# Kernel tuning notes

Measured on AMD Instinct MI355X. Metric: run time of the kernel, lower is better.

## Reference

```python
import jax, jax.numpy as jnp
import numpy as np

B, S, D_MODEL, D_SPACE, N, TOP_K = 4, 2048, 2048, 64, 512, 8


def topk_sparsify(weights, k):
    # weights: [..., N] softmax probs -> keep top-k, renormalize
    topk_vals, topk_idx = jax.lax.top_k(weights, k)
    n = weights.shape[-1]
    one_hot = jax.nn.one_hot(topk_idx, n, dtype=weights.dtype)  # [..., k, N]
    sparse = (one_hot * topk_vals[..., None]).sum(axis=-2)
    return sparse / (sparse.sum(axis=-1, keepdims=True) + 1e-8)


def setup_inputs() -> dict:
    key = jax.random.key(0)
    k1, k2, k3, k4 = jax.random.split(key, 4)
    total = 4 * N + 2 * 256  # fqk + fv + rqk + rv + fknow + rknow
    return {
        "x": jax.random.normal(k1, (B, S, D_MODEL), jnp.float32),
        "W_all": jax.random.normal(k2, (D_MODEL, 6 * D_SPACE), jnp.float32) * 0.02,
        "b_all": jnp.zeros((6 * D_SPACE,), jnp.float32),
        "neuron_emb": jax.random.normal(k3, (total, D_SPACE), jnp.float32) * 0.02,
    }


def reference(x, W_all, b_all, neuron_emb):
    # deterministic=True path: dropout is identity
    emb = neuron_emb / (jnp.linalg.norm(neuron_emb, axis=-1, keepdims=True) + 1e-8)
    h = jnp.einsum('bsd,de->bse', x, W_all) + b_all  # [B,S,6*d_space]
    hs = jnp.split(h, 6, axis=-1)  # fqk_Q, fqk_K, fv, rqk_Q, rqk_K, rv
    # embedding segments: fqk, fv, rqk, rv (each N wide)
    segs = [emb[0:N], emb[0:N], emb[N:2 * N], emb[2 * N:3 * N], emb[2 * N:3 * N], emb[3 * N:4 * N]]
    prefs = [jax.nn.softmax(jnp.einsum('bsd,nd->bsn', hi, ei), axis=-1)
             for hi, ei in zip(hs, segs)]
    # load-balance aux loss: sum over circuits of N * sum((mean_usage - 1/N)^2)
    target = 1.0 / N
    aux_loss = jnp.float32(0.0)
    for p in prefs:
        usage = p.mean(axis=(0, 1))
        aux_loss = aux_loss + ((usage - target) ** 2).sum() * N
    weights = jnp.stack([topk_sparsify(p, TOP_K) for p in prefs], axis=0)  # [6,B,S,N]
    return weights, aux_loss
```

## Files before the change

### kernel.cpp

```cpp
#include <hip/hip_runtime.h>
#include <hip/hip_bf16.h>
#include <math.h>

#define NC   6
#define NN   512
#define DSP  64
#define MTOK 8192
#define DM   2048
#define HN   384
#define NROWS (NC * MTOK)
#define CAP  2048
#define TAU  2e-4f
#define LGP  17
#define NCPY 16

typedef __attribute__((ext_vector_type(8))) short  bf16x8;
typedef __attribute__((ext_vector_type(4))) float  f32x4;
typedef unsigned short ushort_t;

__device__ __forceinline__ float wsumf(float v) {
#pragma unroll
  for (int m = 32; m >= 1; m >>= 1) v += __shfl_xor(v, m, 64);
  return v;
}
__device__ __forceinline__ double wsumd(double v) {
#pragma unroll
  for (int m = 32; m >= 1; m >>= 1) v += __shfl_xor(v, m, 64);
  return v;
}
__device__ __forceinline__ double wmaxd(double v) {
#pragma unroll
  for (int m = 32; m >= 1; m >>= 1) v = fmax(v, __shfl_xor(v, m, 64));
  return v;
}
__device__ __forceinline__ int wmini(int v) {
#pragma unroll
  for (int m = 32; m >= 1; m >>= 1) v = min(v, __shfl_xor(v, m, 64));
  return v;
}
__device__ __forceinline__ void wmaxf2(float& a, float& b) {
#pragma unroll
  for (int m = 32; m >= 1; m >>= 1) {
    float ta = __shfl_xor(a, m, 64);
    float tb = __shfl_xor(b, m, 64);
    a = fmaxf(a, ta);
    b = fmaxf(b, tb);
  }
}
__device__ __forceinline__ void wsumf2(float& a, float& b) {
#pragma unroll
  for (int m = 32; m >= 1; m >>= 1) {
    float ta = __shfl_xor(a, m, 64);
    float tb = __shfl_xor(b, m, 64);
    a += ta;
    b += tb;
  }
}
__device__ __forceinline__ void bf16split(float f, ushort_t& hi, ushort_t& lo) {
  __hip_bfloat16 hb = __float2bfloat16(f);
  float hf = __bfloat162float(hb);
  __hip_bfloat16 lb = __float2bfloat16(f - hf);
  hi = *(ushort_t*)&hb;
  lo = *(ushort_t*)&lb;
}

__global__ __launch_bounds__(256) void k_norm_emb(const float* __restrict__ emb,
                                                  float* __restrict__ embn32,
                                                  double* __restrict__ embn64) {
  int row  = blockIdx.x * 4 + (threadIdx.x >> 6);
  int lane = threadIdx.x & 63;
  double v = (double)emb[(size_t)row * DSP + lane];
  double ss = wsumd(v * v);
  double inv = 1.0 / (sqrt(ss) + 1e-8);
  double o = v * inv;
  embn64[(size_t)row * DSP + lane] = o;
  embn32[(size_t)row * DSP + lane] = (float)o;
}

__global__ __launch_bounds__(256) void k_split_x(const float* __restrict__ X,
                                                 ushort_t* __restrict__ xhi,
                                                 ushort_t* __restrict__ xlo) {
  const size_t t = (size_t)blockIdx.x * 256 + threadIdx.x;
  const int lane = (int)(t & 63);
  const int s    = (int)((t >> 6) & 63);
  const int g    = (int)(t >> 12);
  const int m = (g << 4) + (lane & 15);
  const int k = (s << 5) + (((lane >> 4) & 3) << 3);
  const float* xp = &X[(size_t)m * DM + k];
  ushort_t h8[8], l8[8];
#pragma unroll
  for (int j = 0; j < 8; j++) bf16split(xp[j], h8[j], l8[j]);
  *(bf16x8*)&xhi[t * 8] = *(bf16x8*)h8;
  *(bf16x8*)&xlo[t * 8] = *(bf16x8*)l8;
}

__global__ __launch_bounds__(256) void k_split_w(const float* __restrict__ W,
                                                 ushort_t* __restrict__ whi,
                                                 ushort_t* __restrict__ wlo) {
  const size_t t = (size_t)blockIdx.x * 256 + threadIdx.x;
  const int lane = (int)(t & 63);
  const int s    = (int)((t >> 6) & 63);
  const int Hb   = (int)(t >> 12);
  const int n = (Hb << 4) + (lane & 15);
  const int k = (s << 5) + (((lane >> 4) & 3) << 3);
  ushort_t h8[8], l8[8];
#pragma unroll
  for (int j = 0; j < 8; j++) bf16split(W[(size_t)(k + j) * HN + n], h8[j], l8[j]);
  *(bf16x8*)&whi[t * 8] = *(bf16x8*)h8;
  *(bf16x8*)&wlo[t * 8] = *(bf16x8*)l8;
}

__global__ __launch_bounds__(256) void k_gemm_mfma(const ushort_t* __restrict__ xhi,
                                                   const ushort_t* __restrict__ xlo,
                                                   const ushort_t* __restrict__ whi,
                                                   const ushort_t* __restrict__ wlo,
                                                   const float* __restrict__ Bv,
                                                   float* __restrict__ H) {
  __shared__ bf16x8 Bs[2][8][64];
  const int tid = threadIdx.x, lane = tid & 63, w = tid >> 6;
  const int Gw  = blockIdx.x * 8 + w * 2;
  const int Hb0 = blockIdx.y * 4;
  const bf16x8* XH = (const bf16x8*)xhi;
  const bf16x8* XL = (const bf16x8*)xlo;
  const bf16x8* WH = (const bf16x8*)whi;
  const bf16x8* WL = (const bf16x8*)wlo;

#define FIDX(G, s) (((size_t)(G) * 64 + (s)) * 64 + lane)

  f32x4 acc[2][4];
#pragma unroll
  for (int i = 0; i < 2; i++)
#pragma unroll
    for (int j = 0; j < 4; j++) acc[i][j] = (f32x4){0.f, 0.f, 0.f, 0.f};

  {
    const int p0 = w, p1 = w + 4;
    Bs[0][p0][lane] = ((p0 & 1) ? WL : WH)[FIDX(Hb0 + (p0 >> 1), 0)];
    Bs[0][p1][lane] = ((p1 & 1) ? WL : WH)[FIDX(Hb0 + (p1 >> 1), 0)];
  }
  __syncthreads();

  for (int s = 0; s < 64; s++) {
    const int buf = s & 1;
    if (s < 63) {
      const int p0 = w, p1 = w + 4, nb = buf ^ 1;
      Bs[nb][p0][lane] = ((p0 & 1) ? WL : WH)[FIDX(Hb0 + (p0 >> 1), s + 1)];
      Bs[nb][p1][lane] = ((p1 & 1) ? WL : WH)[FIDX(Hb0 + (p1 >> 1), s + 1)];
    }
    const bf16x8 ah0 = XH[FIDX(Gw, s)],     al0 = XL[FIDX(Gw, s)];
    const bf16x8 ah1 = XH[FIDX(Gw + 1, s)], al1 = XL[FIDX(Gw + 1, s)];
#pragma unroll
    for (int j = 0; j < 4; j++) {
      const bf16x8 bh = Bs[buf][j * 2][lane];
      const bf16x8 bl = Bs[buf][j * 2 + 1][lane];
      acc[0][j] = __builtin_amdgcn_mfma_f32_16x16x32_bf16(ah0, bh, acc[0][j], 0, 0, 0);
      acc[0][j] = __builtin_amdgcn_mfma_f32_16x16x32_bf16(ah0, bl, acc[0][j], 0, 0, 0);
      acc[0][j] = __builtin_amdgcn_mfma_f32_16x16x32_bf16(al0, bh, acc[0][j], 0, 0, 0);
      acc[1][j] = __builtin_amdgcn_mfma_f32_16x16x32_bf16(ah1, bh, acc[1][j], 0, 0, 0);
      acc[1][j] = __builtin_amdgcn_mfma_f32_16x16x32_bf16(ah1, bl, acc[1][j], 0, 0, 0);
      acc[1][j] = __builtin_amdgcn_mfma_f32_16x16x32_bf16(al1, bh, acc[1][j], 0, 0, 0);
    }
    __syncthreads();
  }

#pragma unroll
  for (int i = 0; i < 2; i++)
#pragma unroll
    for (int j = 0; j < 4; j++) {
      const int col = (Hb0 + j) * 16 + (lane & 15);
      const float bias = Bv[col];
#pragma unroll
      for (int r = 0; r < 4; r++) {
        const int row = (Gw + i) * 16 + ((lane >> 4) << 2) + r;
        H[(size_t)row * HN + col] = acc[i][j][r] + bias;
      }
    }
#undef FIDX
}

__global__ __launch_bounds__(256) void k_split_h(const float* __restrict__ H,
                                                 ushort_t* __restrict__ hfh,
                                                 ushort_t* __restrict__ hfl) {
  const size_t t = (size_t)blockIdx.x * 256 + threadIdx.x;
  const int lane = (int)(t & 63);
  const int ks   = (int)((t >> 6) & 1);
  const int g    = (int)((t >> 7) & 511);
  const int c    = (int)(t >> 16);
  const int m = g * 16 + (lane & 15);
  const int col = c * 64 + ks * 32 + (((lane >> 4) & 3) << 3);
  const float* hp = &H[(size_t)m * HN + col];
  ushort_t h8[8], l8[8];
#pragma unroll
  for (int j = 0; j < 8; j++) bf16split(hp[j], h8[j], l8[j]);
  *(bf16x8*)&hfh[t * 8] = *(bf16x8*)h8;
  *(bf16x8*)&hfl[t * 8] = *(bf16x8*)l8;
}

__global__ __launch_bounds__(256) void k_split_e(const float* __restrict__ E,
                                                 ushort_t* __restrict__ efh,
                                                 ushort_t* __restrict__ efl) {
  const size_t t = (size_t)blockIdx.x * 256 + threadIdx.x;
  const int lane = (int)(t & 63);
  const int ks   = (int)((t >> 6) & 1);
  const int ng   = (int)((t >> 7) & 31);
  const int seg  = (int)(t >> 12);
  const int n = seg * 512 + ng * 16 + (lane & 15);
  const int k = ks * 32 + (((lane >> 4) & 3) << 3);
  const float* ep = &E[(size_t)n * DSP + k];
  ushort_t h8[8], l8[8];
#pragma unroll
  for (int j = 0; j < 8; j++) bf16split(ep[j], h8[j], l8[j]);
  *(bf16x8*)&efh[t * 8] = *(bf16x8*)h8;
  *(bf16x8*)&efl[t * 8] = *(bf16x8*)l8;
}

__global__ __launch_bounds__(512, 3) void k_router_mfma(const ushort_t* __restrict__ hfh,
                                                        const ushort_t* __restrict__ hfl,
                                                        const ushort_t* __restrict__ efh,
                                                        const ushort_t* __restrict__ efl,
                                                        float* __restrict__ OUT,
                                                        float* __restrict__ UC,
                                                        int* __restrict__ ncand,
                                                        int* __restrict__ cand_rows) {
  __shared__ float lgT[NN * LGP];
  const int tid  = threadIdx.x;
  const int lane = tid & 63;
  const int wid  = tid >> 6;
  const int g    = blockIdx.x;
  const int c    = blockIdx.y;
  const int segb = (c <= 1) ? 0 : (c == 2) ? 512 : (c == 5) ? 1536 : 1024;
  const int seg  = segb >> 9;

  const bf16x8* HH = (const bf16x8*)hfh;
  const bf16x8* HL = (const bf16x8*)hfl;
  const bf16x8* EH = (const bf16x8*)efh;
  const bf16x8* EL = (const bf16x8*)efl;

  const size_t ab = ((size_t)(c * 512 + g) * 2) * 64 + lane;
  const bf16x8 ah0 = HH[ab], ah1 = HH[ab + 64];
  const bf16x8 al0 = HL[ab], al1 = HL[ab + 64];

#pragma unroll
  for (int ng = 0; ng < 4; ng++) {
    const int ngg = wid * 4 + ng;
    const size_t bb = ((size_t)(seg * 32 + ngg) * 2) * 64 + lane;
    const bf16x8 bh0 = EH[bb], bh1 = EH[bb + 64];
    const bf16x8 bl0 = EL[bb], bl1 = EL[bb + 64];
    f32x4 a = (f32x4){0.f, 0.f, 0.f, 0.f};
    a = __builtin_amdgcn_mfma_f32_16x16x32_bf16(ah0, bh0, a, 0, 0, 0);
    a = __builtin_amdgcn_mfma_f32_16x16x32_bf16(ah0, bl0, a, 0, 0, 0);
    a = __builtin_amdgcn_mfma_f32_16x16x32_bf16(al0, bh0, a, 0, 0, 0);
    a = __builtin_amdgcn_mfma_f32_16x16x32_bf16(ah1, bh1, a, 0, 0, 0);
    a = __builtin_amdgcn_mfma_f32_16x16x32_bf16(ah1, bl1, a, 0, 0, 0);
    a = __builtin_amdgcn_mfma_f32_16x16x32_bf16(al1, bh1, a, 0, 0, 0);
    const int n  = wid * 64 + ng * 16 + (lane & 15);
    const int tb = (lane >> 4) << 2;
#pragma unroll
    for (int r = 0; r < 4; r++) lgT[n * LGP + tb + r] = a[r];
  }
  __syncthreads();

  const int tA = wid * 2, tB = tA + 1;
  const int rowA = c * MTOK + g * 16 + tA;
  const int rowB = rowA + 1;

  float vA[8], eA[8], vB[8], eB[8];
#pragma unroll
  for (int k = 0; k < 8; k++) {
    vA[k] = lgT[(lane + 64 * k) * LGP + tA];
    vB[k] = lgT[(lane + 64 * k) * LGP + tB];
    eA[k] = __expf(vA[k]);
    eB[k] = __expf(vB[k]);
  }
  float sA = ((eA[0] + eA[1]) + (eA[2] + eA[3])) + ((eA[4] + eA[5]) + (eA[6] + eA[7]));
  float sB = ((eB[0] + eB[1]) + (eB[2] + eB[3])) + ((eB[4] + eB[5]) + (eB[6] + eB[7]));
  wsumf2(sA, sB);

  float w8A[8], w8B[8];
#pragma unroll
  for (int k = 0; k < 8; k++) { w8A[k] = 0.f; w8B[k] = 0.f; }
  float M7A = 0.f, M7B = 0.f;

#pragma unroll
  for (int it = 0; it < 8; it++) {
    float mA = vA[0]; int iA = 0;
    float mB = vB[0]; int iB = 0;
#pragma unroll
    for (int k = 1; k < 8; k++) {
      bool gA = vA[k] > mA; iA = gA ? k : iA; mA = gA ? vA[k] : mA;
      bool gB = vB[k] > mB; iB = gB ? k : iB; mB = gB ? vB[k] : mB;
    }
    float MA = mA, MB = mB;
    wmaxf2(MA, MB);
    unsigned long long balA = __ballot(mA == MA);
    unsigned long long balB = __ballot(mB == MB);
    const bool winA = (lane == __ffsll(balA) - 1);
    const bool winB = (lane == __ffsll(balB) - 1);
#pragma unroll
    for (int k = 0; k < 8; k++) {
      bool uA = winA && (iA == k);
      bool uB = winB && (iB == k);
      w8A[k] = uA ? eA[k] : w8A[k];
      vA[k]  = uA ? -INFINITY : vA[k];
      w8B[k] = uB ? eB[k] : w8B[k];
      vB[k]  = uB ? -INFINITY : vB[k];
    }
    if (it == 7) { M7A = MA; M7B = MB; }
  }
  {
    float mA = vA[0], mB = vB[0];
#pragma unroll
    for (int k = 1; k < 8; k++) { mA = fmaxf(mA, vA[k]); mB = fmaxf(mB, vB[k]); }
    wmaxf2(mA, mB);
    if (lane == 0) {
      if ((M7A - mA) < TAU) {
        int ci = atomicAdd(ncand, 1);
        if (ci < CAP) cand_rows[ci] = rowA;
      }
      if ((M7B - mB) < TAU) {
        int ci = atomicAdd(ncand, 1);
        if (ci < CAP) cand_rows[ci] = rowB;
      }
    }
  }
  float d8A = ((w8A[0] + w8A[1]) + (w8A[2] + w8A[3])) + ((w8A[4] + w8A[5]) + (w8A[6] + w8A[7]));
  float d8B = ((w8B[0] + w8B[1]) + (w8B[2] + w8B[3])) + ((w8B[4] + w8B[5]) + (w8B[6] + w8B[7]));
  wsumf2(d8A, d8B);
  const float invA = 1.0f / (d8A + 1e-8f * sA), rcpsA = 1.0f / sA;
  const float invB = 1.0f / (d8B + 1e-8f * sB), rcpsB = 1.0f / sB;
  float* outA = OUT + (size_t)rowA * NN;
  float* outB = OUT + (size_t)rowB * NN;
  float uacc[8];
#pragma unroll
  for (int k = 0; k < 8; k++) {
    uacc[k] = fmaf(eA[k], rcpsA, 0.f);
    uacc[k] = fmaf(eB[k], rcpsB, uacc[k]);
    outA[lane + 64 * k] = w8A[k] * invA;
    outB[lane + 64 * k] = w8B[k] * invB;
  }

  __syncthreads();
  float* uw = lgT;
#pragma unroll
  for (int k = 0; k < 8; k++) uw[wid * NN + lane + 64 * k] = uacc[k];
  __syncthreads();
  {
    float a = 0.f;
#pragma unroll
    for (int w = 0; w < 8; w++) a += uw[w * NN + tid];
    atomicAdd(&UC[((size_t)(blockIdx.x & (NCPY - 1)) * NC + c) * NN + tid], a);
  }
}

__global__ __launch_bounds__(512) void k_gemm(const float* __restrict__ X,
                                              const float* __restrict__ W,
                                              const float* __restrict__ Bv,
                                              float* __restrict__ H) {
  __shared__ float As[32][133];
  __shared__ float Bs[32][68];
  const int tid = threadIdx.x;
  const int tx = tid & 15, ty = tid >> 4;
  const int m0 = blockIdx.x * 128, n0 = blockIdx.y * 64;
  float acc[16];
#pragma unroll
  for (int i = 0; i < 16; i++) acc[i] = 0.f;
  const int am = tid >> 2, aq = (tid & 3) * 2;
  const int bk = tid >> 4, bn = tid & 15;
  for (int k0 = 0; k0 < DM; k0 += 32) {
#pragma unroll
    for (int p = 0; p < 2; p++) {
      float4 a4 = *(const float4*)&X[(size_t)(m0 + am) * DM + k0 + (aq + p) * 4];
      As[(aq + p) * 4 + 0][am] = a4.x; As[(aq + p) * 4 + 1][am] = a4.y;
      As[(aq + p) * 4 + 2][am] = a4.z; As[(aq + p) * 4 + 3][am] = a4.w;
    }
    {
      float4 b4 = *(const float4*)&W[(size_t)(k0 + bk) * HN + n0 + bn * 4];
      *(float4*)&Bs[bk][bn * 4] = b4;
    }
    __syncthreads();
#pragma unroll
    for (int kk = 0; kk < 32; kk++) {
      float4 a4 = *(const float4*)&As[kk][ty * 4];
      float4 b4 = *(const float4*)&Bs[kk][tx * 4];
      acc[ 0] = fmaf(a4.x, b4.x, acc[ 0]); acc[ 1] = fmaf(a4.x, b4.y, acc[ 1]);
      acc[ 2] = fmaf(a4.x, b4.z, acc[ 2]); acc[ 3] = fmaf(a4.x, b4.w, acc[ 3]);
      acc[ 4] = fmaf(a4.y, b4.x, acc[ 4]); acc[ 5] = fmaf(a4.y, b4.y, acc[ 5]);
      acc[ 6] = fmaf(a4.y, b4.z, acc[ 6]); acc[ 7] = fmaf(a4.y, b4.w, acc[ 7]);
      acc[ 8] = fmaf(a4.z, b4.x, acc[ 8]); acc[ 9] = fmaf(a4.z, b4.y, acc[ 9]);
      acc[10] = fmaf(a4.z, b4.z, acc[10]); acc[11] = fmaf(a4.z, b4.w, acc[11]);
      acc[12] = fmaf(a4.w, b4.x, acc[12]); acc[13] = fmaf(a4.w, b4.y, acc[13]);
      acc[14] = fmaf(a4.w, b4.z, acc[14]); acc[15] = fmaf(a4.w, b4.w, acc[15]);
    }
    __syncthreads();
  }
#pragma unroll
  for (int i = 0; i < 4; i++) {
    const int row = m0 + ty * 4 + i;
    const int col = n0 + tx * 4;
    float4 o;
    o.x = acc[i*4+0] + Bv[col + 0];
    o.y = acc[i*4+1] + Bv[col + 1];
    o.z = acc[i*4+2] + Bv[col + 2];
    o.w = acc[i*4+3] + Bv[col + 3];
    *(float4*)&H[(size_t)row * HN + col] = o;
  }
}

__global__ __launch_bounds__(512, 3) void k_router(const float* __restrict__ H,
                                                   const float* __restrict__ EMB,
                                                   float* __restrict__ OUT,
                                                   float* __restrict__ UC,
                                                   int* __restrict__ ncand,
                                                   int* __restrict__ cand_rows) {
  __shared__ float lg[16][NN];
  const int tid  = threadIdx.x;
  const int lane = tid & 63;
  const int wid  = tid >> 6;
  const int c    = blockIdx.y;
  const int t0   = blockIdx.x * 16;
  const int segb = (c <= 1) ? 0 : (c == 2) ? 512 : (c == 5) ? 1536 : 1024;
  const int nidx = wid * 64 + lane;
  const int erow = segb + nidx;

  float lgacc[16];
#pragma unroll
  for (int t = 0; t < 16; t++) lgacc[t] = 0.f;

#pragma unroll
  for (int half = 0; half < 2; half++) {
    const float4* ep = (const float4*)&EMB[(size_t)erow * DSP + half * 32];
    const float4 e0 = ep[0], e1 = ep[1], e2 = ep[2], e3 = ep[3];
    const float4 e4 = ep[4], e5 = ep[5], e6 = ep[6], e7 = ep[7];
#pragma unroll
    for (int t = 0; t < 16; t++) {
      const float4* h4 = (const float4*)&H[(size_t)(t0 + t) * HN + c * DSP + half * 32];
      const float4 h0 = h4[0], h1 = h4[1], h2 = h4[2], h3 = h4[3];
      const float4 h4_ = h4[4], h5 = h4[5], h6 = h4[6], h7 = h4[7];
      float a = 0.f, b = 0.f;
      a = fmaf(h0.x, e0.x, a); a = fmaf(h0.y, e0.y, a); a = fmaf(h0.z, e0.z, a); a = fmaf(h0.w, e0.w, a);
      b = fmaf(h1.x, e1.x, b); b = fmaf(h1.y, e1.y, b); b = fmaf(h1.z, e1.z, b); b = fmaf(h1.w, e1.w, b);
      a = fmaf(h2.x, e2.x, a); a = fmaf(h2.y, e2.y, a); a = fmaf(h2.z, e2.z, a); a = fmaf(h2.w, e2.w, a);
      b = fmaf(h3.x, e3.x, b); b = fmaf(h3.y, e3.y, b); b = fmaf(h3.z, e3.z, b); b = fmaf(h3.w, e3.w, b);
      a = fmaf(h4_.x, e4.x, a); a = fmaf(h4_.y, e4.y, a); a = fmaf(h4_.z, e4.z, a); a = fmaf(h4_.w, e4.w, a);
      b = fmaf(h5.x, e5.x, b); b = fmaf(h5.y, e5.y, b); b = fmaf(h5.z, e5.z, b); b = fmaf(h5.w, e5.w, b);
      a = fmaf(h6.x, e6.x, a); a = fmaf(h6.y, e6.y, a); a = fmaf(h6.z, e6.z, a); a = fmaf(h6.w, e6.w, a);
      b = fmaf(h7.x, e7.x, b); b = fmaf(h7.y, e7.y, b); b = fmaf(h7.z, e7.z, b); b = fmaf(h7.w, e7.w, b);
      lgacc[t] += a + b;
    }
  }
#pragma unroll
  for (int t = 0; t < 16; t++) lg[t][nidx] = lgacc[t];
  __syncthreads();

  float uacc[8];
#pragma unroll
  for (int k = 0; k < 8; k++) uacc[k] = 0.f;

#pragma unroll
  for (int r = 0; r < 2; r++) {
    const int t = wid * 2 + r;
    const int row = c * MTOK + t0 + t;
    float vv[8], ex[8];
#pragma unroll
    for (int k = 0; k < 8; k++) {
      vv[k] = lg[t][lane + 64 * k];
      ex[k] = __expf(vv[k]);
    }
    float sl = ((ex[0] + ex[1]) + (ex[2] + ex[3])) + ((ex[4] + ex[5]) + (ex[6] + ex[7]));
    const float s = wsumf(sl);

    float w8[8];
#pragma unroll
    for (int k = 0; k < 8; k++) w8[k] = 0.f;
    float M7 = 0.f;

#pragma unroll
    for (int it = 0; it < 8; it++) {
      float lmaxv = vv[0]; int lidx = 0;
#pragma unroll
      for (int k = 1; k < 8; k++) {
        bool gg = vv[k] > lmaxv;
        lidx  = gg ? k : lidx;
        lmaxv = gg ? vv[k] : lmaxv;
      }
      float M = lmaxv;
#pragma unroll
      for (int m = 32; m >= 1; m >>= 1) M = fmaxf(M, __shfl_xor(M, m, 64));
      unsigned long long bal = __ballot(lmaxv == M);
      const bool win = (lane == __ffsll(bal) - 1);
#pragma unroll
      for (int k = 0; k < 8; k++) {
        bool u = win && (lidx == k);
        w8[k] = u ? ex[k] : w8[k];
        vv[k] = u ? -INFINITY : vv[k];
      }
      if (it == 7) M7 = M;
    }
    {
      float lmaxv = vv[0];
#pragma unroll
      for (int k = 1; k < 8; k++) lmaxv = fmaxf(lmaxv, vv[k]);
#pragma unroll
      for (int m = 32; m >= 1; m >>= 1) lmaxv = fmaxf(lmaxv, __shfl_xor(lmaxv, m, 64));
      if (lane == 0 && (M7 - lmaxv) < TAU) {
        int ci = atomicAdd(ncand, 1);
        if (ci < CAP) cand_rows[ci] = row;
      }
    }
    float d8l = ((w8[0] + w8[1]) + (w8[2] + w8[3])) + ((w8[4] + w8[5]) + (w8[6] + w8[7]));
    const float d8 = wsumf(d8l);
    const float inv  = 1.0f / (d8 + 1e-8f * s);
    const float rcps = 1.0f / s;
    float* outp = OUT + (size_t)row * NN;
#pragma unroll
    for (int k = 0; k < 8; k++) {
      uacc[k] = fmaf(ex[k], rcps, uacc[k]);
      outp[lane + 64 * k] = w8[k] * inv;
    }
  }

  __syncthreads();
  float* uw = (float*)&lg[0][0];
#pragma unroll
  for (int k = 0; k < 8; k++) uw[wid * NN + lane + 64 * k] = uacc[k];
  __syncthreads();
  {
    float a = 0.f;
#pragma unroll
    for (int w = 0; w < 8; w++) a += uw[w * NN + tid];
    atomicAdd(&UC[((size_t)(blockIdx.x & (NCPY - 1)) * NC + c) * NN + tid], a);
  }
}

__global__ __launch_bounds__(512) void k_refine(const float* __restrict__ X,
                                                const float* __restrict__ W,
                                                const float* __restrict__ Bv,
                                                const double* __restrict__ E64,
                                                const int* __restrict__ ncand,
                                                const int* __restrict__ cand_rows,
                                                float* __restrict__ OUT,
                                                int* __restrict__ crow,
                                                double* __restrict__ cgap,
                                                int* __restrict__ cidx9,
                                                float* __restrict__ cex9,
                                                float* __restrict__ cs) {
  const int n = min(*ncand, CAP);
  const int bid = blockIdx.x;
  if (bid >= n) return;
  const int row = cand_rows[bid];
  const int c = row / MTOK, tok = row - c * MTOK;
  const int segb = (c <= 1) ? 0 : (c == 2) ? 512 : (c == 5) ? 1536 : 1024;
  const int tid = threadIdx.x, lane = tid & 63, wid = tid >> 6;

  __shared__ double hred[8][64];
  __shared__ double h64[64];
  __shared__ double lgs[NN];
  __shared__ float  sred[512];
  __shared__ int    sidx[9];
  __shared__ float  sex[9];
  __shared__ double sM[9];

  {
    const float* xb = &X[(size_t)tok * DM + wid * 256];
    const float* wb = &W[(size_t)(wid * 256) * HN + c * DSP + lane];
    double a0 = 0.0, a1 = 0.0;
#pragma unroll 4
    for (int i = 0; i < 256; i += 2) {
      a0 = fma((double)xb[i],     (double)wb[(size_t)i * HN],       a0);
      a1 = fma((double)xb[i + 1], (double)wb[(size_t)(i + 1) * HN], a1);
    }
    hred[wid][lane] = a0 + a1;
  }
  __syncthreads();
  if (tid < 64) {
    double t = ((hred[0][tid] + hred[1][tid]) + (hred[2][tid] + hred[3][tid]))
             + ((hred[4][tid] + hred[5][tid]) + (hred[6][tid] + hred[7][tid]));
    h64[tid] = t + (double)Bv[c * DSP + tid];
  }
  __syncthreads();

  {
    const double* e = &E64[(size_t)(segb + tid) * DSP];
    double a = 0.0;
#pragma unroll
    for (int q = 0; q < 64; q++) a = fma(h64[q], e[q], a);
    lgs[tid] = a;
    sred[tid] = __expf((float)a);
  }
  __syncthreads();
  for (int st = 256; st > 0; st >>= 1) {
    if (tid < st) sred[tid] += sred[tid + st];
    __syncthreads();
  }
  const float s = sred[0];

  if (wid == 0) {
    double vv[8];
#pragma unroll
    for (int k = 0; k < 8; k++) vv[k] = lgs[lane + 64 * k];
#pragma unroll
    for (int it = 0; it < 9; it++) {
      double lmaxv = vv[0]; int lidx = 0;
#pragma unroll
      for (int k = 1; k < 8; k++) {
        bool g = vv[k] > lmaxv;
        lidx  = g ? k : lidx;
        lmaxv = g ? vv[k] : lmaxv;
      }
      const double M = wmaxd(lmaxv);
      int ncnd = (lmaxv == M) ? (lane + (lidx << 6)) : 0x7FFFFFFF;
      const int nsel = wmini(ncnd);
      if (lane == 0) { sidx[it] = nsel; sex[it] = __expf((float)M); sM[it] = M; }
      if (it < 8) {
        const bool win = ((nsel & 63) == lane);
        const int ksel = nsel >> 6;
#pragma unroll
        for (int k = 0; k < 8; k++) {
          bool u = win && (ksel == k);
          vv[k] = u ? -INFINITY : vv[k];
        }
      }
    }
  }
  __syncthreads();

  float d8 = 0.f;
#pragma unroll
  for (int k = 0; k < 8; k++) d8 += sex[k];
  const float inv = 1.0f / (d8 + 1e-8f * s);
  float val = 0.f;
#pragma unroll
  for (int k = 0; k < 8; k++) val = (tid == sidx[k]) ? sex[k] * inv : val;
  OUT[(size_t)row * NN + tid] = val;

  if (tid == 0) { crow[bid] = row; cgap[bid] = sM[7] - sM[8]; cs[bid] = s; }
  if (tid < 9)  { cidx9[bid * 9 + tid] = sidx[tid]; cex9[bid * 9 + tid] = sex[tid]; }
}

__global__ __launch_bounds__(1024) void k_fixup(const int* __restrict__ ncand,
                                                const int* __restrict__ crow,
                                                const double* __restrict__ cgap,
                                                const int* __restrict__ cidx9,
                                                const float* __restrict__ cex9,
                                                const float* __restrict__ cs,
                                                float* __restrict__ OUT) {
  const int n = min(*ncand, CAP);
  __shared__ double g[1024];
  __shared__ int gr[1024], gi[1024];
  const int tid = threadIdx.x;
  double best = 1e300; int brow = 0x7FFFFFFF, bi = -1;
  for (int i = tid; i < n; i += 1024) {
    double v = cgap[i]; int r = crow[i];
    if (v < best || (v == best && r < brow)) { best = v; brow = r; bi = i; }
  }
  g[tid] = best; gr[tid] = brow; gi[tid] = bi;
  __syncthreads();
  for (int st = 512; st > 0; st >>= 1) {
    if (tid < st) {
      if (g[tid + st] < g[tid] || (g[tid + st] == g[tid] && gr[tid + st] < gr[tid])) {
        g[tid] = g[tid + st]; gr[tid] = gr[tid + st]; gi[tid] = gi[tid + st];
      }
    }
    __syncthreads();
  }
  if (tid == 0 && gi[0] >= 0 && g[0] < 1e-4) {
    const int ci = gi[0], row = gr[0];
    float d = 0.f;
    for (int k = 0; k < 7; k++) d += cex9[ci * 9 + k];
    d += cex9[ci * 9 + 8];
    const float inv = 1.0f / (d + 1e-8f * cs[ci]);
    float* o = OUT + (size_t)row * NN;
    o[cidx9[ci * 9 + 7]] = 0.f;
    for (int k = 0; k < 7; k++)
      o[cidx9[ci * 9 + k]] = cex9[ci * 9 + k] * inv;
    o[cidx9[ci * 9 + 8]] = cex9[ci * 9 + 8] * inv;
  }
}

__global__ __launch_bounds__(512) void k_aux(const float* __restrict__ UC,
                                             float* __restrict__ out_aux) {
  __shared__ float red[512];
  const int tid = threadIdx.x;
  float acc = 0.f;
  for (int i = tid; i < NC * NN; i += 512) {
    float a = 0.f;
#pragma unroll
    for (int cp = 0; cp < NCPY; cp++) a += UC[(size_t)cp * NC * NN + i];
    float u = a * (1.0f / 8192.0f);
    float d = u - (1.0f / 512.0f);
    acc += d * d;
  }
  red[tid] = acc;
  __syncthreads();
  for (int s = 256; s > 0; s >>= 1) {
    if (tid < s) red[tid] += red[tid + s];
    __syncthreads();
  }
  if (tid == 0) out_aux[0] = red[0] * 512.0f;
}

extern "C" void kernel_launch(void* const* d_in, const int* in_sizes, int n_in,
                              void* d_out, int out_size, void* d_ws, size_t ws_size,
                              hipStream_t stream) {
  const float* x   = (const float*)d_in[0];
  const float* W   = (const float*)d_in[1];
  const float* b   = (const float*)d_in[2];
  const float* emb = (const float*)d_in[3];
  float* out = (float*)d_out;

  char* ws = (char*)d_ws;
  size_t off = 0;
  float*  embn32 = (float*) (ws + off); off += (size_t)2048 * 64 * 4;
  double* embn64 = (double*)(ws + off); off += (size_t)2048 * 64 * 8;
  float*  h      = (float*) (ws + off); off += (size_t)MTOK * HN * 4;
  float*  ucopy  = (float*) (ws + off); off += (size_t)NCPY * NC * NN * 4;
  int*    ncand  = (int*)   (ws + off); off += 16;
  int* cand_rows = (int*)   (ws + off); off += (size_t)CAP * 4;
  int*    crow   = (int*)   (ws + off); off += (size_t)CAP * 4;
  double* cgap   = (double*)(ws + off); off += (size_t)CAP * 8;
  float*  cs     = (float*) (ws + off); off += (size_t)CAP * 4;
  int*    cidx9  = (int*)   (ws + off); off += (size_t)CAP * 9 * 4;
  float*  cex9   = (float*) (ws + off); off += (size_t)CAP * 9 * 4;
  ushort_t* xhi = (ushort_t*)(ws + off); off += (size_t)MTOK * DM * 2;
  ushort_t* xlo = (ushort_t*)(ws + off); off += (size_t)MTOK * DM * 2;
  ushort_t* whi = (ushort_t*)(ws + off); off += (size_t)DM * HN * 2;
  ushort_t* wlo = (ushort_t*)(ws + off); off += (size_t)DM * HN * 2;
  ushort_t* hfh = (ushort_t*)(ws + off); off += (size_t)MTOK * HN * 2;
  ushort_t* hfl = (ushort_t*)(ws + off); off += (size_t)MTOK * HN * 2;
  ushort_t* efh = (ushort_t*)(ws + off); off += (size_t)2048 * 64 * 2;
  ushort_t* efl = (ushort_t*)(ws + off); off += (size_t)2048 * 64 * 2;
  const size_t need = off;

  hipMemsetAsync(ucopy, 0, (size_t)NCPY * NC * NN * sizeof(float), stream);
  hipMemsetAsync(ncand, 0, sizeof(int), stream);

  k_norm_emb<<<dim3(512), dim3(256), 0, stream>>>(emb, embn32, embn64);

  if (ws_size >= need) {
    k_split_x<<<dim3((MTOK / 16) * (DM / 32) / 4), dim3(256), 0, stream>>>(x, xhi, xlo);
    k_split_w<<<dim3((HN / 16) * (DM / 32) / 4), dim3(256), 0, stream>>>(W, whi, wlo);
    k_gemm_mfma<<<dim3(MTOK / 128, HN / 64), dim3(256), 0, stream>>>(xhi, xlo, whi, wlo, b, h);
    k_split_e<<<dim3(64), dim3(256), 0, stream>>>(embn32, efh, efl);
    k_split_h<<<dim3(1536), dim3(256), 0, stream>>>(h, hfh, hfl);
    k_router_mfma<<<dim3(MTOK / 16, NC), dim3(512), 0, stream>>>(hfh, hfl, efh, efl,
                                                                 out, ucopy, ncand, cand_rows);
  } else {
    k_gemm<<<dim3(MTOK / 128, HN / 64), dim3(512), 0, stream>>>(x, W, b, h);
    k_router<<<dim3(MTOK / 16, NC), dim3(512), 0, stream>>>(h, embn32, out, ucopy,
                                                            ncand, cand_rows);
  }

  k_refine<<<dim3(CAP), dim3(512), 0, stream>>>(x, W, b, embn64, ncand, cand_rows,
                                                out, crow, cgap, cidx9, cex9, cs);
  k_fixup<<<dim3(1), dim3(1024), 0, stream>>>(ncand, crow, cgap, cidx9, cex9, cs, out);
  k_aux<<<dim3(1), dim3(512), 0, stream>>>(ucopy, out + (size_t)NC * MTOK * NN);
}
```

Baseline: 217.4 us.

## Fuse hi/lo bf16 split into GEMM epilogue and use packed-key sorted top-k

The GEMM epilogue now stages each wave's output tile in shared memory and writes the hi/lo bf16 fragment layout directly. This removes the fp32 H intermediate round-trip and the separate k_split_h launch. The router's top-8 selection packs each logit into an order-preserving uint with the slot index in its low 3 bits. It sorts the 8 per-lane values with a compare-exchange network, then pops the lane head per iteration with an integer wave max, instead of rescanning all 8 values. Truncating the low 3 mantissa bits can change tie and near-tie ordering; the candidate/refine path is meant to absorb this.

New measurement: 192.2 us. 1.13x faster.

```diff
diff --git a/kernel.cpp b/kernel.cpp
--- a/kernel.cpp
+++ b/kernel.cpp
@@ -17,6 +17,7 @@
 typedef __attribute__((ext_vector_type(8))) short  bf16x8;
 typedef __attribute__((ext_vector_type(4))) float  f32x4;
 typedef unsigned short ushort_t;
+typedef unsigned int   uint_t;
 
 __device__ __forceinline__ float wsumf(float v) {
 #pragma unroll
@@ -37,15 +38,6 @@
 #pragma unroll
   for (int m = 32; m >= 1; m >>= 1) v = min(v, __shfl_xor(v, m, 64));
   return v;
-}
-__device__ __forceinline__ void wmaxf2(float& a, float& b) {
-#pragma unroll
-  for (int m = 32; m >= 1; m >>= 1) {
-    float ta = __shfl_xor(a, m, 64);
-    float tb = __shfl_xor(b, m, 64);
-    a = fmaxf(a, ta);
-    b = fmaxf(b, tb);
-  }
 }
 __device__ __forceinline__ void wsumf2(float& a, float& b) {
 #pragma unroll
@@ -54,6 +46,15 @@
     float tb = __shfl_xor(b, m, 64);
     a += ta;
     b += tb;
+  }
+}
+__device__ __forceinline__ void wmaxu2(uint_t& a, uint_t& b) {
+#pragma unroll
+  for (int m = 32; m >= 1; m >>= 1) {
+    uint_t ta = (uint_t)__shfl_xor((int)a, m, 64);
+    uint_t tb = (uint_t)__shfl_xor((int)b, m, 64);
+    a = max(a, ta);
+    b = max(b, tb);
   }
 }
 __device__ __forceinline__ void bf16split(float f, ushort_t& hi, ushort_t& lo) {
@@ -62,6 +63,14 @@
   __hip_bfloat16 lb = __float2bfloat16(f - hf);
   hi = *(ushort_t*)&hb;
   lo = *(ushort_t*)&lb;
+}
+__device__ __forceinline__ uint_t f2sort(float f) {
+  uint_t u = __float_as_uint(f);
+  return u ^ (uint_t)(((int)u >> 31) | 0x80000000);
+}
+__device__ __forceinline__ float sort2f(uint_t s) {
+  uint_t b = (s & 0x80000000u) ? (s ^ 0x80000000u) : ~s;
+  return __uint_as_float(b);
 }
 
 __global__ __launch_bounds__(256) void k_norm_emb(const float* __restrict__ emb,
@@ -115,11 +124,14 @@
                                                    const ushort_t* __restrict__ whi,
                                                    const ushort_t* __restrict__ wlo,
                                                    const float* __restrict__ Bv,
-                                                   float* __restrict__ H) {
+                                                   ushort_t* __restrict__ hfh,
+                                                   ushort_t* __restrict__ hfl) {
   __shared__ bf16x8 Bs[2][8][64];
+  __shared__ float  hw[4][32][65];
   const int tid = threadIdx.x, lane = tid & 63, w = tid >> 6;
   const int Gw  = blockIdx.x * 8 + w * 2;
   const int Hb0 = blockIdx.y * 4;
+  const int cidx = blockIdx.y;
   const bf16x8* XH = (const bf16x8*)xhi;
   const bf16x8* XL = (const bf16x8*)xlo;
   const bf16x8* WH = (const bf16x8*)whi;
@@ -167,33 +179,31 @@
   for (int i = 0; i < 2; i++)
 #pragma unroll
     for (int j = 0; j < 4; j++) {
-      const int col = (Hb0 + j) * 16 + (lane & 15);
-      const float bias = Bv[col];
+      const int colg = Hb0 * 16 + j * 16 + (lane & 15);
+      const float bias = Bv[colg];
+      const int cl = j * 16 + (lane & 15);
 #pragma unroll
       for (int r = 0; r < 4; r++) {
-        const int row = (Gw + i) * 16 + ((lane >> 4) << 2) + r;
-        H[(size_t)row * HN + col] = acc[i][j][r] + bias;
-      }
+        const int rl = i * 16 + ((lane >> 4) << 2) + r;
+        hw[w][rl][cl] = acc[i][j][r] + bias;
+      }
+    }
+#pragma unroll
+  for (int i = 0; i < 2; i++)
+#pragma unroll
+    for (int ks = 0; ks < 2; ks++) {
+      float v8[8];
+#pragma unroll
+      for (int j = 0; j < 8; j++)
+        v8[j] = hw[w][i * 16 + (lane & 15)][ks * 32 + (lane >> 4) * 8 + j];
+      ushort_t h8[8], l8[8];
+#pragma unroll
+      for (int j = 0; j < 8; j++) bf16split(v8[j], h8[j], l8[j]);
+      const size_t t = (((size_t)(cidx * 512 + Gw + i)) * 2 + ks) * 64 + lane;
+      *(bf16x8*)&hfh[t * 8] = *(bf16x8*)h8;
+      *(bf16x8*)&hfl[t * 8] = *(bf16x8*)l8;
     }
 #undef FIDX
-}
-
-__global__ __launch_bounds__(256) void k_split_h(const float* __restrict__ H,
-                                                 ushort_t* __restrict__ hfh,
-                                                 ushort_t* __restrict__ hfl) {
-  const size_t t = (size_t)blockIdx.x * 256 + threadIdx.x;
-  const int lane = (int)(t & 63);
-  const int ks   = (int)((t >> 6) & 1);
-  const int g    = (int)((t >> 7) & 511);
-  const int c    = (int)(t >> 16);
-  const int m = g * 16 + (lane & 15);
-  const int col = c * 64 + ks * 32 + (((lane >> 4) & 3) << 3);
-  const float* hp = &H[(size_t)m * HN + col];
-  ushort_t h8[8], l8[8];
-#pragma unroll
-  for (int j = 0; j < 8; j++) bf16split(hp[j], h8[j], l8[j]);
-  *(bf16x8*)&hfh[t * 8] = *(bf16x8*)h8;
-  *(bf16x8*)&hfl[t * 8] = *(bf16x8*)l8;
 }
 
 __global__ __launch_bounds__(256) void k_split_e(const float* __restrict__ E,
@@ -264,64 +274,73 @@
   const int rowA = c * MTOK + g * 16 + tA;
   const int rowB = rowA + 1;
 
-  float vA[8], eA[8], vB[8], eB[8];
+  float eA[8], eB[8];
+  uint_t pA[8], pB[8];
 #pragma unroll
   for (int k = 0; k < 8; k++) {
-    vA[k] = lgT[(lane + 64 * k) * LGP + tA];
-    vB[k] = lgT[(lane + 64 * k) * LGP + tB];
-    eA[k] = __expf(vA[k]);
-    eB[k] = __expf(vB[k]);
+    float vA = lgT[(lane + 64 * k) * LGP + tA];
+    float vB = lgT[(lane + 64 * k) * LGP + tB];
+    eA[k] = __expf(vA);
+    eB[k] = __expf(vB);
+    pA[k] = (f2sort(vA) & ~7u) | (uint_t)k;
+    pB[k] = (f2sort(vB) & ~7u) | (uint_t)k;
   }
   float sA = ((eA[0] + eA[1]) + (eA[2] + eA[3])) + ((eA[4] + eA[5]) + (eA[6] + eA[7]));
   float sB = ((eB[0] + eB[1]) + (eB[2] + eB[3])) + ((eB[4] + eB[5]) + (eB[6] + eB[7]));
   wsumf2(sA, sB);
 
-  float w8A[8], w8B[8];
-#pragma unroll
-  for (int k = 0; k < 8; k++) { w8A[k] = 0.f; w8B[k] = 0.f; }
-  float M7A = 0.f, M7B = 0.f;
-
+#define CE(P, a, b) { uint_t mx = max(P[a], P[b]); uint_t mn = min(P[a], P[b]); P[a] = mx; P[b] = mn; }
+#define CE2(a, b) CE(pA, a, b) CE(pB, a, b)
+  CE2(0,1) CE2(2,3) CE2(4,5) CE2(6,7)
+  CE2(0,2) CE2(1,3) CE2(4,6) CE2(5,7)
+  CE2(1,2) CE2(5,6)
+  CE2(0,4) CE2(1,5) CE2(2,6) CE2(3,7)
+  CE2(2,4) CE2(3,5)
+  CE2(1,2) CE2(3,4) CE2(5,6)
+#undef CE2
+#undef CE
+
+  uint_t maskA = 0, maskB = 0;
+  uint_t m7A = 0, m7B = 0;
 #pragma unroll
   for (int it = 0; it < 8; it++) {
-    float mA = vA[0]; int iA = 0;
-    float mB = vB[0]; int iB = 0;
-#pragma unroll
-    for (int k = 1; k < 8; k++) {
-      bool gA = vA[k] > mA; iA = gA ? k : iA; mA = gA ? vA[k] : mA;
-      bool gB = vB[k] > mB; iB = gB ? k : iB; mB = gB ? vB[k] : mB;
-    }
-    float MA = mA, MB = mB;
-    wmaxf2(MA, MB);
-    unsigned long long balA = __ballot(mA == MA);
-    unsigned long long balB = __ballot(mB == MB);
+    const uint_t hA = pA[0], hB = pB[0];
+    uint_t MA = hA, MB = hB;
+    wmaxu2(MA, MB);
+    unsigned long long balA = __ballot(hA == MA);
+    unsigned long long balB = __ballot(hB == MB);
     const bool winA = (lane == __ffsll(balA) - 1);
     const bool winB = (lane == __ffsll(balB) - 1);
-#pragma unroll
-    for (int k = 0; k < 8; k++) {
-      bool uA = winA && (iA == k);
-      bool uB = winB && (iB == k);
-      w8A[k] = uA ? eA[k] : w8A[k];
-      vA[k]  = uA ? -INFINITY : vA[k];
-      w8B[k] = uB ? eB[k] : w8B[k];
-      vB[k]  = uB ? -INFINITY : vB[k];
-    }
-    if (it == 7) { M7A = MA; M7B = MB; }
+    maskA = winA ? (maskA | (1u << (MA & 7u))) : maskA;
+    maskB = winB ? (maskB | (1u << (MB & 7u))) : maskB;
+#pragma unroll
+    for (int k = 0; k < 7; k++) {
+      pA[k] = winA ? pA[k + 1] : pA[k];
+      pB[k] = winB ? pB[k + 1] : pB[k];
+    }
+    pA[7] = winA ? 0u : pA[7];
+    pB[7] = winB ? 0u : pB[7];
+    if (it == 7) { m7A = MA; m7B = MB; }
   }
   {
-    float mA = vA[0], mB = vB[0];
-#pragma unroll
-    for (int k = 1; k < 8; k++) { mA = fmaxf(mA, vA[k]); mB = fmaxf(mB, vB[k]); }
-    wmaxf2(mA, mB);
+    uint_t MA = pA[0], MB = pB[0];
+    wmaxu2(MA, MB);
     if (lane == 0) {
-      if ((M7A - mA) < TAU) {
+      if ((sort2f(m7A & ~7u) - sort2f(MA & ~7u)) < TAU) {
         int ci = atomicAdd(ncand, 1);
         if (ci < CAP) cand_rows[ci] = rowA;
       }
-      if ((M7B - mB) < TAU) {
+      if ((sort2f(m7B & ~7u) - sort2f(MB & ~7u)) < TAU) {
         int ci = atomicAdd(ncand, 1);
         if (ci < CAP) cand_rows[ci] = rowB;
       }
     }
+  }
+  float w8A[8], w8B[8];
+#pragma unroll
+  for (int k = 0; k < 8; k++) {
+    w8A[k] = (maskA & (1u << k)) ? eA[k] : 0.f;
+    w8B[k] = (maskB & (1u << k)) ? eB[k] : 0.f;
   }
   float d8A = ((w8A[0] + w8A[1]) + (w8A[2] + w8A[3])) + ((w8A[4] + w8A[5]) + (w8A[6] + w8A[7]));
   float d8B = ((w8B[0] + w8B[1]) + (w8B[2] + w8B[3])) + ((w8B[4] + w8B[5]) + (w8B[6] + w8B[7]));
@@ -739,9 +758,9 @@
   if (ws_size >= need) {
     k_split_x<<<dim3((MTOK / 16) * (DM / 32) / 4), dim3(256), 0, stream>>>(x, xhi, xlo);
     k_split_w<<<dim3((HN / 16) * (DM / 32) / 4), dim3(256), 0, stream>>>(W, whi, wlo);
-    k_gemm_mfma<<<dim3(MTOK / 128, HN / 64), dim3(256), 0, stream>>>(xhi, xlo, whi, wlo, b, h);
     k_split_e<<<dim3(64), dim3(256), 0, stream>>>(embn32, efh, efl);
-    k_split_h<<<dim3(1536), dim3(256), 0, stream>>>(h, hfh, hfl);
+    k_gemm_mfma<<<dim3(MTOK / 128, HN / 64), dim3(256), 0, stream>>>(xhi, xlo, whi, wlo,
+                                                                     b, hfh, hfl);
     k_router_mfma<<<dim3(MTOK / 16, NC), dim3(512), 0, stream>>>(hfh, hfl, efh, efl,
                                                                  out, ucopy, ncand, cand_rows);
   } else {
```
